# Kernel optimization log

Hardware: AMD Instinct MI355X
Metric: run time of the kernel (lower is better)

The kernel has to match this reference:

```python
import jax, jax.numpy as jnp
import numpy as np

HEAD = 16

def setup_inputs() -> dict:
    key = jax.random.key(0)
    k1, k2, k3 = jax.random.split(key, 3)
    B, S, D = 2, 2048, 1024
    x = jax.random.normal(k1, (B, S, D), dtype=jnp.float32)
    w_qkv = jax.random.normal(k2, (D, 3 * D), dtype=jnp.float32) * (1.0 / np.sqrt(D))
    b_qkv = jnp.zeros((3 * D,), dtype=jnp.float32)
    w_out = jax.random.normal(k3, (D, D), dtype=jnp.float32) * (1.0 / np.sqrt(D))
    b_out = jnp.zeros((D,), dtype=jnp.float32)
    return {"x": x, "w_qkv": w_qkv, "b_qkv": b_qkv, "w_out": w_out, "b_out": b_out}


def reference(x, w_qkv, b_qkv, w_out, b_out):
    B, S, D = x.shape
    hd = D // HEAD  # head dim
    qkv = x @ w_qkv + b_qkv                      # [B,S,3D]
    qkv = qkv.reshape(B, S, 3, HEAD, hd)
    qkv = jnp.transpose(qkv, (2, 0, 3, 1, 4))    # [3,B,H,S,hd]
    q, k, v = qkv[0], qkv[1], qkv[2]
    scores = jnp.einsum('bhqd,bhkd->bhqk', q, k)  # [B,H,S,S]
    causal = jnp.triu(jnp.ones((S, S), dtype=bool), k=1)
    scores = jnp.where(causal, -jnp.inf, scores)
    scores = scores / jnp.sqrt(jnp.asarray(hd, dtype=x.dtype))
    attn = jax.nn.softmax(scores, axis=-1)
    z = jnp.einsum('bhqk,bhkd->bhqd', attn, v)   # [B,H,S,hd]
    z = jnp.transpose(z, (0, 2, 1, 3)).reshape(B, S, D)
    out = z @ w_out + b_out
    return out
```

## Files before the change

kernel.cpp:

```cpp
#include <hip/hip_runtime.h>

#define S_LEN  2048
#define NH     16
#define HD     64
#define DMODEL 1024

using bf16x8 = __attribute__((ext_vector_type(8))) __bf16;
using f32x4  = __attribute__((ext_vector_type(4))) float;

__device__ __forceinline__ unsigned short f2bf(float f) {
    unsigned u = __float_as_uint(f);
    u += 0x7FFFu + ((u >> 16) & 1u);
    return (unsigned short)(u >> 16);
}
__device__ __forceinline__ unsigned pk_trunc(float lo, float hi) {
    return __builtin_amdgcn_perm(__float_as_uint(hi), __float_as_uint(lo), 0x07060302u);
}

#define EXP2(x) __builtin_amdgcn_exp2f(x)

#define GLDS16(gsrc, ldst) \
    __builtin_amdgcn_global_load_lds((__attribute__((address_space(1))) void*)(gsrc), \
                                     (__attribute__((address_space(3))) void*)(ldst), 16, 0, 0)

#define WAIT_LGKM0() __builtin_amdgcn_s_waitcnt(0xC07F)

#define ASM_VMCNT(n)  asm volatile("s_waitcnt vmcnt(" #n ")" ::: "memory")
#define ASM_BARRIER() asm volatile("s_barrier" ::: "memory")

__global__ __launch_bounds__(256) void prep_kernel(
    const float* __restrict__ x, const float* __restrict__ w_qkv,
    const float* __restrict__ w_out,
    unsigned short* __restrict__ xb, unsigned short* __restrict__ wqkvT,
    unsigned short* __restrict__ woutT) {
    __shared__ float T[32][33];
    int bx = blockIdx.x;
    if (bx < 4096) {
        int idx = (bx * 256 + threadIdx.x) * 4;
        float4 v = *(const float4*)(x + idx);
        ushort4 o;
        o.x = f2bf(v.x); o.y = f2bf(v.y); o.z = f2bf(v.z); o.w = f2bf(v.w);
        *(ushort4*)(xb + idx) = o;
        return;
    }
    int tb = bx - 4096;
    int tcol = tb & 127, krow = tb >> 7;
    const float* in;
    unsigned short* out;
    int N, nbx;
    if (tcol < 96) { in = w_qkv; out = wqkvT; N = 3072; nbx = tcol; }
    else           { in = w_out; out = woutT; N = 1024; nbx = tcol - 96; }
    int r  = threadIdx.x >> 3;
    int c4 = (threadIdx.x & 7) * 4;
    int kbase = krow * 32, nbase = nbx * 32;
    float4 v = *(const float4*)(in + (size_t)(kbase + r) * N + nbase + c4);
    T[r][c4 + 0] = v.x; T[r][c4 + 1] = v.y; T[r][c4 + 2] = v.z; T[r][c4 + 3] = v.w;
    __syncthreads();
    ushort4 o;
    o.x = f2bf(T[c4 + 0][r]); o.y = f2bf(T[c4 + 1][r]);
    o.z = f2bf(T[c4 + 2][r]); o.w = f2bf(T[c4 + 3][r]);
    *(ushort4*)(out + (size_t)(nbase + r) * 1024 + kbase + c4) = o;
}

template <int NI, int NT>
__device__ __forceinline__ void mfma_mainloop64(const unsigned short* __restrict__ A,
                                                const unsigned short* __restrict__ B,
                                                int m0, int n0,
                                                unsigned short* As, unsigned short* Bs,
                                                f32x4 acc[4][NI]) {
    constexpr int K = NT * 64;
    const int lane = threadIdx.x & 63, wave = threadIdx.x >> 6;
    const int quad = lane >> 4, l15 = lane & 15;
    const int wm0 = (wave >> 1) * 64, wn0 = (wave & 1) * (NI * 16);

    auto stageA = [&](int t) {
        unsigned short* Ad = As + (t % 3) * 8192;
        #pragma unroll
        for (int j = 0; j < 4; ++j) {
            int c0 = j * 256 + wave * 64;
            int c  = c0 + lane;
            int r = c >> 3, pc = c & 7, q = pc ^ (r & 7);
            GLDS16(A + (size_t)(m0 + r) * K + t * 64 + q * 8, Ad + c0 * 8);
        }
    };
    auto stageB = [&](int t) {
        unsigned short* Bd = Bs + (t & 1) * (NI * 2048);
        #pragma unroll
        for (int j = 0; j < NI; ++j) {
            int c0 = j * 256 + wave * 64;
            int c  = c0 + lane;
            int r = c >> 3, pc = c & 7, q = pc ^ (r & 7);
            GLDS16(B + (size_t)(n0 + r) * K + t * 64 + q * 8, Bd + c0 * 8);
        }
    };

    stageB(0); stageA(0);
    stageB(1); stageA(1);
    stageA(2);

    #pragma unroll
    for (int t = 0; t < NT; ++t) {
        if (t < NT - 1) { ASM_VMCNT(4); } else { ASM_VMCNT(0); }
        ASM_BARRIER();
        if (t >= 1) {
            if (t + 1 < NT) stageB(t + 1);
            if (t + 2 < NT) stageA(t + 2);
        }

        const unsigned short* Ab = As + (t % 3) * 8192;
        const unsigned short* Bb = Bs + (t & 1) * (NI * 2048);
        bf16x8 af[2][4], bfr[2][NI];
        #pragma unroll
        for (int mi = 0; mi < 4; ++mi) {
            int r = wm0 + mi * 16 + l15, x = r & 7;
            af[0][mi] = *(const bf16x8*)(Ab + r * 64 + ((quad    ) ^ x) * 8);
            af[1][mi] = *(const bf16x8*)(Ab + r * 64 + ((4 + quad) ^ x) * 8);
        }
        #pragma unroll
        for (int ni = 0; ni < NI; ++ni) {
            int r = wn0 + ni * 16 + l15, x = r & 7;
            bfr[0][ni] = *(const bf16x8*)(Bb + r * 64 + ((quad    ) ^ x) * 8);
            bfr[1][ni] = *(const bf16x8*)(Bb + r * 64 + ((4 + quad) ^ x) * 8);
        }
        #pragma unroll
        for (int h = 0; h < 2; ++h)
            #pragma unroll
            for (int mi = 0; mi < 4; ++mi)
                #pragma unroll
                for (int ni = 0; ni < NI; ++ni)
                    acc[mi][ni] = __builtin_amdgcn_mfma_f32_16x16x32_bf16(
                        af[h][mi], bfr[h][ni], acc[mi][ni], 0, 0, 0);
    }
}

__global__ __launch_bounds__(256) void gemm_qkv_kernel(
    const unsigned short* __restrict__ xb, const unsigned short* __restrict__ wT,
    const float* __restrict__ bias,
    unsigned short* __restrict__ Qt, unsigned short* __restrict__ Kh,
    unsigned short* __restrict__ Vt) {
    __shared__ __align__(16) unsigned short Sh[40960];
    unsigned short* As = Sh;
    unsigned short* Bs = Sh + 24576;

    f32x4 acc[4][4];
    #pragma unroll
    for (int i = 0; i < 4; ++i)
        #pragma unroll
        for (int j = 0; j < 4; ++j) acc[i][j] = (f32x4){0.f, 0.f, 0.f, 0.f};

    const int bid = blockIdx.x;
    const int xcd = bid & 7, slot = bid >> 3;
    const int nt = xcd * 3 + (slot % 3);
    const int mt = slot / 3;
    const int m0 = mt * 128, n0 = nt * 128;
    mfma_mainloop64<4, 16>(xb, wT, m0, n0, As, Bs, acc);

    const int lane = threadIdx.x & 63, wave = threadIdx.x >> 6;
    const int quad = lane >> 4, l15 = lane & 15;
    const int wm0 = (wave >> 1) * 64, wn0 = (wave & 1) * 64;

    const int colbase = n0 + wn0;
    const int t = colbase >> 10;
    const int h = (colbase >> 6) & (NH - 1);
    const float qscale = (t == 0) ? 0.125f * 1.44269504088896f : 1.0f;
    float bv[4];
    #pragma unroll
    for (int ni = 0; ni < 4; ++ni) bv[ni] = bias[colbase + ni * 16 + l15];

    __syncthreads();
    unsigned short* Lw = Sh + wave * 1536;

    #pragma unroll
    for (int mi = 0; mi < 4; ++mi) {
        int mbase = m0 + wm0 + mi * 16;
        int b = mbase >> 11, sbase = mbase & (S_LEN - 1);
        if (t == 1) {
            #pragma unroll
            for (int ni = 0; ni < 4; ++ni)
                #pragma unroll
                for (int r = 0; r < 4; ++r)
                    Lw[(quad * 4 + r) * 72 + ni * 16 + l15] =
                        f2bf(acc[mi][ni][r] + bv[ni]);
            WAIT_LGKM0();
            int rr = lane & 15, dc = (lane >> 4) * 16;
            uint4 v0 = *(const uint4*)(Lw + rr * 72 + dc);
            uint4 v1 = *(const uint4*)(Lw + rr * 72 + dc + 8);
            unsigned short* dst =
                Kh + ((size_t)(b * NH + h) * S_LEN + sbase + rr) * HD + dc;
            *(uint4*)dst = v0;
            *(uint4*)(dst + 8) = v1;
        } else {
            #pragma unroll
            for (int ni = 0; ni < 4; ++ni)
                #pragma unroll
                for (int r = 0; r < 4; ++r)
                    Lw[(ni * 16 + l15) * 24 + quad * 4 + r] =
                        f2bf((acc[mi][ni][r] + bv[ni]) * qscale);
            WAIT_LGKM0();
            int c = lane;
            uint4 v0 = *(const uint4*)(Lw + c * 24);
            uint4 v1 = *(const uint4*)(Lw + c * 24 + 8);
            unsigned short* base = (t == 0) ? Qt : Vt;
            unsigned short* dst =
                base + ((size_t)(b * NH + h) * HD + c) * S_LEN + sbase;
            *(uint4*)dst = v0;
            *(uint4*)(dst + 8) = v1;
        }
        WAIT_LGKM0();
    }
}

__global__ __launch_bounds__(256) void gemm_out_kernel(
    const unsigned short* __restrict__ zb, const unsigned short* __restrict__ wT,
    const float* __restrict__ bias, float* __restrict__ out) {
    __shared__ __align__(16) unsigned short As[24576], Bs[8192];
    f32x4 acc[4][2];
    #pragma unroll
    for (int i = 0; i < 4; ++i)
        #pragma unroll
        for (int j = 0; j < 2; ++j) acc[i][j] = (f32x4){0.f, 0.f, 0.f, 0.f};

    const int bid = blockIdx.x;
    const int xcd = bid & 7, slot = bid >> 3;
    const int nt = xcd * 2 + (slot & 1);
    const int mt = slot >> 1;
    const int m0 = mt * 128, n0 = nt * 64;
    mfma_mainloop64<2, 16>(zb, wT, m0, n0, As, Bs, acc);

    const int lane = threadIdx.x & 63, wave = threadIdx.x >> 6;
    const int quad = lane >> 4, l15 = lane & 15;
    const int wm0 = (wave >> 1) * 64, wn0 = (wave & 1) * 32;
    #pragma unroll
    for (int mi = 0; mi < 4; ++mi) {
        #pragma unroll
        for (int ni = 0; ni < 2; ++ni) {
            int col = n0 + wn0 + ni * 16 + l15;
            float bvv = bias[col];
            #pragma unroll
            for (int r = 0; r < 4; ++r)
                out[(size_t)(m0 + wm0 + mi * 16 + quad * 4 + r) * DMODEL + col] =
                    acc[mi][ni][r] + bvv;
        }
    }
}

__device__ const int g_sched[24 * 4] = {
    15,0,15,0,  15,16,31,1,  7,0,15,-1,
    14,0,14,0,  14,15,29,1,  6,0,13,-1,
    13,0,13,0,  13,14,27,1,
    12,0,12,0,  12,13,25,1,  5,0,11,-1,
    11,0,11,0,  11,12,23,1,
    10,0,10,0,  10,11,21,1,  4,0,9,-1,
     9,0,9,0,    9,10,19,1,
     8,0,8,0,    8,9,17,1,   3,0,7,-1,
     2,0,5,-1,   1,0,3,-1,   0,0,1,-1
};

__global__ __launch_bounds__(512) void attn_mfma_kernel(
    const unsigned short* __restrict__ Qt, const unsigned short* __restrict__ Kh,
    const unsigned short* __restrict__ Vt, unsigned short* __restrict__ zb,
    float* __restrict__ Zp, float* __restrict__ lp) {
    __shared__ __align__(16) unsigned short Ks[2 * 64 * 64];
    __shared__ __align__(16) unsigned short Vs[2 * 64 * 64];
    __shared__ __align__(16) unsigned short Pl[8 * 16 * 64];

    const int lane = threadIdx.x & 63, wave = threadIdx.x >> 6;
    const int quad = lane >> 4, l15 = lane & 15;
    const int bh = blockIdx.x;
    const int qt   = g_sched[blockIdx.y * 4 + 0];
    const int klo  = g_sched[blockIdx.y * 4 + 1];
    const int khi  = g_sched[blockIdx.y * 4 + 2];
    const int part = g_sched[blockIdx.y * 4 + 3];
    const int q0 = qt * 128;
    const float M0 = 12.0f;

    bf16x8 qf0, qf1;
    {
        const unsigned short* qb = Qt + (size_t)bh * HD * S_LEN + q0 + wave * 16 + l15;
        union { bf16x8 v; unsigned short u[8]; } u0, u1;
        #pragma unroll
        for (int j = 0; j < 8; ++j) {
            u0.u[j] = qb[(quad * 8 + j) * S_LEN];
            u1.u[j] = qb[(32 + quad * 8 + j) * S_LEN];
        }
        qf0 = u0.v; qf1 = u1.v;
    }

    f32x4 Z[4];
    #pragma unroll
    for (int i = 0; i < 4; ++i) Z[i] = (f32x4){0.f, 0.f, 0.f, 0.f};
    float rsum = 0.f;

    unsigned short* pw = Pl + wave * 1024;
    const int pwrow = l15 * 64;

    auto stageKV = [&](int kt, int b) {
        {
            int c0 = wave * 64;
            int c  = c0 + lane;
            int r = c >> 3, pc = c & 7, q = pc ^ (r & 7);
            GLDS16(Kh + ((size_t)bh * S_LEN + kt * 64 + r) * HD + q * 8,
                   Ks + b * 4096 + c0 * 8);
        }
        {
            int c0 = wave * 64;
            int c  = c0 + lane;
            int d = c >> 3, pc = c & 7, q = pc ^ (d & 7);
            GLDS16(Vt + ((size_t)bh * HD + d) * S_LEN + kt * 64 + q * 8,
                   Vs + b * 4096 + c0 * 8);
        }
    };

    auto body = [&](int kt, int cb, bool pref) {
        if (pref) {
            stageKV(kt + 1, cb ^ 1);
            ASM_VMCNT(2);
        } else {
            ASM_VMCNT(0);
        }
        ASM_BARRIER();

        const unsigned short* Kb = Ks + cb * 4096;
        const unsigned short* Vb = Vs + cb * 4096;

        const int kq = kt - 2 * qt;
        const int dw = (kq >= 0) ? (wave - (kq << 2)) : 7;
        if (dw >= 0) {
            const int nmax = dw < 3 ? dw : 3;
            const int qthr = dw * 16 + l15 - quad * 4;

            #pragma unroll
            for (int n = 0; n < 4; ++n) {
                int woff = pwrow + (((2 * n + (quad >> 1)) ^ (l15 & 7)) << 3) + (quad & 1) * 4;
                if (n <= nmax) {
                    int rk = n * 16 + l15;
                    int x = rk & 7;
                    bf16x8 kv0 = *(const bf16x8*)(Kb + rk * 64 + ((quad    ) ^ x) * 8);
                    bf16x8 kv1 = *(const bf16x8*)(Kb + rk * 64 + ((4 + quad) ^ x) * 8);
                    f32x4 t4 = (f32x4){-M0, -M0, -M0, -M0};
                    __builtin_amdgcn_s_setprio(1);
                    t4 = __builtin_amdgcn_mfma_f32_16x16x32_bf16(kv0, qf0, t4, 0, 0, 0);
                    t4 = __builtin_amdgcn_mfma_f32_16x16x32_bf16(kv1, qf1, t4, 0, 0, 0);
                    __builtin_amdgcn_s_setprio(0);
                    float p[4];
                    #pragma unroll
                    for (int r = 0; r < 4; ++r) {
                        p[r] = EXP2(t4[r]);
                        if ((n * 16 + r) > qthr) p[r] = 0.f;
                        rsum += p[r];
                    }
                    uint2 pk;
                    pk.x = pk_trunc(p[0], p[1]);
                    pk.y = pk_trunc(p[2], p[3]);
                    *(uint2*)(pw + woff) = pk;
                } else {
                    *(uint2*)(pw + woff) = (uint2){0u, 0u};
                }
            }

            const int khmax = (dw >> 1) < 1 ? (dw >> 1) : 1;
            for (int kh = 0; kh <= khmax; ++kh) {
                bf16x8 pa = *(const bf16x8*)(pw + pwrow + ((kh * 4 + quad) ^ (l15 & 7)) * 8);
                __builtin_amdgcn_s_setprio(1);
                #pragma unroll
                for (int ni = 0; ni < 4; ++ni) {
                    int rd = ni * 16 + l15;
                    bf16x8 vb = *(const bf16x8*)(Vb + rd * 64 + ((kh * 4 + quad) ^ (rd & 7)) * 8);
                    Z[ni] = __builtin_amdgcn_mfma_f32_16x16x32_bf16(vb, pa, Z[ni], 0, 0, 0);
                }
                __builtin_amdgcn_s_setprio(0);
            }
        }
        ASM_BARRIER();
    };

    stageKV(klo, 0);
    {
        int cnt = khi - klo + 1;
        int kt = klo;
        while (cnt >= 2) {
            body(kt, 0, true);
            body(kt + 1, 1, cnt > 2);
            kt += 2; cnt -= 2;
        }
        if (cnt == 1) body(kt, 0, false);
    }

    rsum += __shfl_xor(rsum, 16);
    rsum += __shfl_xor(rsum, 32);

    const int ql = wave * 16 + l15;
    if (part < 0) {
        const int b = bh >> 4, h = bh & (NH - 1);
        float inv = 1.f / rsum;
        size_t rowoff = (size_t)(b * S_LEN + q0 + ql) * DMODEL + h * HD;
        #pragma unroll
        for (int ni = 0; ni < 4; ++ni) {
            ushort4 o;
            o.x = f2bf(Z[ni][0] * inv);
            o.y = f2bf(Z[ni][1] * inv);
            o.z = f2bf(Z[ni][2] * inv);
            o.w = f2bf(Z[ni][3] * inv);
            *(ushort4*)(zb + rowoff + ni * 16 + quad * 4) = o;
        }
    } else {
        const int slot = (qt - 8) * 2 + part;
        float* zpo = Zp + ((size_t)(slot * 32 + bh) * 128 + ql) * 64;
        #pragma unroll
        for (int ni = 0; ni < 4; ++ni) {
            float4 st;
            st.x = Z[ni][0]; st.y = Z[ni][1]; st.z = Z[ni][2]; st.w = Z[ni][3];
            *(float4*)(zpo + ni * 16 + quad * 4) = st;
        }
        if (quad == 0)
            lp[(size_t)(slot * 32 + bh) * 128 + ql] = rsum;
    }
}

__global__ __launch_bounds__(256) void attn_merge_kernel(
    const float* __restrict__ Zp, const float* __restrict__ lp,
    unsigned short* __restrict__ zb) {
    const int bh = blockIdx.x, qi = blockIdx.y, qt = 8 + qi;
    const int t = threadIdx.x;
    const int q = t >> 1;
    const int d0 = (t & 1) << 5;
    const int s0 = qi * 2, s1 = s0 + 1;
    float l = lp[(size_t)(s0 * 32 + bh) * 128 + q] +
              lp[(size_t)(s1 * 32 + bh) * 128 + q];
    float inv = 1.f / l;
    const float* z0 = Zp + ((size_t)(s0 * 32 + bh) * 128 + q) * 64 + d0;
    const float* z1 = Zp + ((size_t)(s1 * 32 + bh) * 128 + q) * 64 + d0;
    const int b = bh >> 4, h = bh & (NH - 1);
    unsigned short* o =
        zb + (size_t)(b * S_LEN + qt * 128 + q) * DMODEL + h * HD + d0;
    #pragma unroll
    for (int i = 0; i < 32; i += 4) {
        float4 a = *(const float4*)(z0 + i);
        float4 c = *(const float4*)(z1 + i);
        ushort4 ov;
        ov.x = f2bf((a.x + c.x) * inv);
        ov.y = f2bf((a.y + c.y) * inv);
        ov.z = f2bf((a.z + c.z) * inv);
        ov.w = f2bf((a.w + c.w) * inv);
        *(ushort4*)(o + i) = ov;
    }
}

extern "C" void kernel_launch(void* const* d_in, const int* in_sizes, int n_in,
                              void* d_out, int out_size, void* d_ws, size_t ws_size,
                              hipStream_t stream)
{
    const float* x     = (const float*)d_in[0];
    const float* w_qkv = (const float*)d_in[1];
    const float* b_qkv = (const float*)d_in[2];
    const float* w_out = (const float*)d_in[3];
    const float* b_out = (const float*)d_in[4];
    float* out = (float*)d_out;

    unsigned short* wsu   = (unsigned short*)d_ws;
    unsigned short* xb    = wsu;
    unsigned short* wqkvT = xb    + (size_t)4194304;
    unsigned short* woutT = wqkvT + (size_t)3145728;
    unsigned short* Qt    = woutT + (size_t)1048576;
    unsigned short* Kh    = Qt    + (size_t)4194304;
    unsigned short* Vt    = Kh    + (size_t)4194304;
    unsigned short* zb    = Vt    + (size_t)4194304;
    float* Zp = (float*)(zb + (size_t)4194304);
    float* lp = Zp + (size_t)16 * 32 * 128 * 64;

    prep_kernel<<<dim3(8192), 256, 0, stream>>>(x, w_qkv, w_out, xb, wqkvT, woutT);

    gemm_qkv_kernel<<<dim3(768), 256, 0, stream>>>(
        xb, wqkvT, b_qkv, Qt, Kh, Vt);

    attn_mfma_kernel<<<dim3(2 * NH, 24), 512, 0, stream>>>(Qt, Kh, Vt, zb, Zp, lp);
    attn_merge_kernel<<<dim3(2 * NH, 8), 256, 0, stream>>>(Zp, lp, zb);

    gemm_out_kernel<<<dim3(512), 256, 0, stream>>>(
        zb, woutT, b_out, out);
}
```

Measured before the change: 169.0 us.

## Triple-buffer K/V tiles and drop the trailing barrier per iteration

Moves the K/V shared-memory staging from double to triple buffering. The prefetch of tile kt+2 is issued after the top-of-iteration barrier, so the end-of-body barrier can be removed. This is meant to halve the barriers per K tile and keep two tile loads in flight while computing. It costs more LDS per block, which may lower occupancy, and it makes the prologue and remainder handling more involved.

```diff
diff --git a/kernel.cpp b/kernel.cpp
--- a/kernel.cpp
+++ b/kernel.cpp
@@ -260,8 +260,8 @@
     const unsigned short* __restrict__ Qt, const unsigned short* __restrict__ Kh,
     const unsigned short* __restrict__ Vt, unsigned short* __restrict__ zb,
     float* __restrict__ Zp, float* __restrict__ lp) {
-    __shared__ __align__(16) unsigned short Ks[2 * 64 * 64];
-    __shared__ __align__(16) unsigned short Vs[2 * 64 * 64];
+    __shared__ __align__(16) unsigned short Ks[3 * 64 * 64];
+    __shared__ __align__(16) unsigned short Vs[3 * 64 * 64];
     __shared__ __align__(16) unsigned short Pl[8 * 16 * 64];
 
     const int lane = threadIdx.x & 63, wave = threadIdx.x >> 6;
@@ -311,14 +311,10 @@
         }
     };
 
-    auto body = [&](int kt, int cb, bool pref) {
-        if (pref) {
-            stageKV(kt + 1, cb ^ 1);
-            ASM_VMCNT(2);
-        } else {
-            ASM_VMCNT(0);
-        }
+    auto body = [&](int kt, int cb, bool notlast, bool pref, int pkt, int dst) {
+        if (notlast) { ASM_VMCNT(2); } else { ASM_VMCNT(0); }
         ASM_BARRIER();
+        if (pref) stageKV(pkt, dst);
 
         const unsigned short* Kb = Ks + cb * 4096;
         const unsigned short* Vb = Vs + cb * 4096;
@@ -371,19 +367,27 @@
                 __builtin_amdgcn_s_setprio(0);
             }
         }
-        ASM_BARRIER();
     };
 
-    stageKV(klo, 0);
     {
-        int cnt = khi - klo + 1;
-        int kt = klo;
-        while (cnt >= 2) {
-            body(kt, 0, true);
-            body(kt + 1, 1, cnt > 2);
-            kt += 2; cnt -= 2;
-        }
-        if (cnt == 1) body(kt, 0, false);
+        const int n = khi - klo + 1;
+        stageKV(klo, 0);
+        if (n > 1) stageKV(klo + 1, 1);
+        int i = 0;
+        while (n - i >= 3) {
+            bool g3 = (n - i) > 3, g4 = (n - i) > 4;
+            body(klo + i,     0, true, true, klo + i + 2, 2);
+            body(klo + i + 1, 1, true, g3,   klo + i + 3, 0);
+            body(klo + i + 2, 2, g3,   g4,   klo + i + 4, 1);
+            i += 3;
+        }
+        int r = n - i;
+        if (r == 2) {
+            body(klo + i,     0, true,  false, 0, 0);
+            body(klo + i + 1, 1, false, false, 0, 0);
+        } else if (r == 1) {
+            body(klo + i,     0, false, false, 0, 0);
+        }
     }
 
     rsum += __shfl_xor(rsum, 16);
```

New measurement: 178.3 us. +5.5%, slower.
